# Kernel tuning notes

Hardware: AMD Instinct MI355X
Metric: run time of the kernel (lower is better)

The kernel has to match this reference:

```python
import jax, jax.numpy as jnp
import numpy as np

N = 50000      # nodes
DEG = 16       # fixed neighbors per node
F = 128        # feat_dim
E = N * DEG    # edges
EPS = 1e-12


def setup_inputs() -> dict:
    key = jax.random.key(0)
    k_x, k_col = jax.random.split(key)
    x = jax.random.normal(k_x, (N, F), dtype=jnp.float32)
    col_id = jax.random.randint(k_col, (E,), 0, N, dtype=jnp.int32)
    row_ptr = (jnp.arange(N + 1, dtype=jnp.int32) * DEG)          # CSR offsets, fixed degree
    row_id = jnp.repeat(jnp.arange(N, dtype=jnp.int32), DEG)      # COO row index per edge
    beta = jnp.ones((1,), dtype=jnp.float32)
    return {"x": x, "row_id": row_id, "row_ptr": row_ptr, "col_id": col_id, "beta": beta}


def reference(x, row_id, row_ptr, col_id, beta):
    # AGNN: alpha_ij = softmax_j( beta * cos(x_i, x_j) ), out_i = sum_j alpha_ij * x_j
    n = x.shape[0]
    xn = x * jax.lax.rsqrt(jnp.sum(x * x, axis=-1, keepdims=True) + EPS)   # row-normalized
    # per-edge cosine similarity scaled by beta
    e = beta[0] * jnp.sum(xn[row_id] * xn[col_id], axis=-1)                # [E]
    # segment softmax over each row's neighborhood
    m = jax.ops.segment_max(e, row_id, num_segments=n)                      # [N]
    ee = jnp.exp(e - m[row_id])
    s = jax.ops.segment_sum(ee, row_id, num_segments=n)                     # [N]
    alpha = ee / s[row_id]                                                  # [E]
    # attention-weighted aggregation of raw neighbor features
    out = jax.ops.segment_sum(alpha[:, None] * x[col_id], row_id, num_segments=n)  # [N, F]
    return out
```

## Files before the change

kernel.cpp:

```cpp
#include <hip/hip_runtime.h>
#include <math.h>
#include <stdint.h>

#define DEG 16
#define FDIM 128
#define EPSV 1e-12f

__device__ __forceinline__ uint32_t f32_to_bf16_rne(float f) {
    uint32_t u = __float_as_uint(f);
    return (u + 0x7fffu + ((u >> 16) & 1u)) >> 16;
}

__device__ __forceinline__ void unpack8(const uint4 u, float* f) {
    f[0] = __uint_as_float(u.x << 16); f[1] = __uint_as_float(u.x & 0xffff0000u);
    f[2] = __uint_as_float(u.y << 16); f[3] = __uint_as_float(u.y & 0xffff0000u);
    f[4] = __uint_as_float(u.z << 16); f[5] = __uint_as_float(u.z & 0xffff0000u);
    f[6] = __uint_as_float(u.w << 16); f[7] = __uint_as_float(u.w & 0xffff0000u);
}

__global__ void agnn_prep_kernel(const float* __restrict__ x,
                                 uint32_t* __restrict__ xbf,
                                 float* __restrict__ rn, int n) {
    int wave = (blockIdx.x * blockDim.x + threadIdx.x) >> 6;
    int lane = threadIdx.x & 63;
    if (wave >= n) return;
    const float2 v = *reinterpret_cast<const float2*>(x + (size_t)wave * FDIM + lane * 2);
    float s = v.x * v.x + v.y * v.y;
#pragma unroll
    for (int off = 32; off >= 1; off >>= 1)
        s += __shfl_xor(s, off);
    if (lane == 0) rn[wave] = rsqrtf(s + EPSV);
    xbf[(size_t)wave * (FDIM / 2) + lane] =
        f32_to_bf16_rne(v.x) | (f32_to_bf16_rne(v.y) << 16);
}

__global__ void agnn_main_v3(const uint32_t* __restrict__ xbf,
                             const int* __restrict__ col_id,
                             const float* __restrict__ rn,
                             const float* __restrict__ beta,
                             float* __restrict__ out, int n) {
    int wave = (blockIdx.x * blockDim.x + threadIdx.x) >> 6;
    int lane = threadIdx.x & 63;
    if (wave >= n) return;
    const int node = wave;
    const int g = lane >> 4;
    const int t = lane & 15;

    const float b   = beta[0];
    const float rni = rn[node];

    const uint4 xiu = *reinterpret_cast<const uint4*>(xbf + (size_t)node * (FDIM / 2) + t * 4);
    float xi[8];
    unpack8(xiu, xi);

    const int call = col_id[node * DEG + t];

    int   cj[4];
    uint4 xju[4];
#pragma unroll
    for (int r = 0; r < 4; ++r) {
        cj[r]  = __shfl(call, 4 * g + r);
        xju[r] = *reinterpret_cast<const uint4*>(xbf + (size_t)cj[r] * (FDIM / 2) + t * 4);
    }
    float rnj[4];
#pragma unroll
    for (int r = 0; r < 4; ++r) rnj[r] = rn[cj[r]];

    float p[4];
#pragma unroll
    for (int r = 0; r < 4; ++r) {
        float xv[8];
        unpack8(xju[r], xv);
        float d0 = xi[0] * xv[0];
        float d1 = xi[1] * xv[1];
#pragma unroll
        for (int q = 2; q < 8; q += 2) {
            d0 = fmaf(xi[q],     xv[q],     d0);
            d1 = fmaf(xi[q + 1], xv[q + 1], d1);
        }
        p[r] = d0 + d1;
    }

#pragma unroll
    for (int off = 1; off < 16; off <<= 1) {
#pragma unroll
        for (int r = 0; r < 4; ++r)
            p[r] += __shfl_xor(p[r], off);
    }

    const float brni = b * rni;
#pragma unroll
    for (int r = 0; r < 4; ++r)
        p[r] *= brni * rnj[r];

    float m = fmaxf(fmaxf(p[0], p[1]), fmaxf(p[2], p[3]));
    m = fmaxf(m, __shfl_xor(m, 16));
    m = fmaxf(m, __shfl_xor(m, 32));
    float s = 0.f;
#pragma unroll
    for (int r = 0; r < 4; ++r) { p[r] = __expf(p[r] - m); s += p[r]; }
    s += __shfl_xor(s, 16);
    s += __shfl_xor(s, 32);
    const float inv = 1.0f / s;

    float acc[8] = {0.f, 0.f, 0.f, 0.f, 0.f, 0.f, 0.f, 0.f};
#pragma unroll
    for (int r = 0; r < 4; ++r) {
        const float a = p[r] * inv;
        float xv[8];
        unpack8(xju[r], xv);
#pragma unroll
        for (int q = 0; q < 8; ++q)
            acc[q] = fmaf(a, xv[q], acc[q]);
    }
#pragma unroll
    for (int q = 0; q < 8; ++q) acc[q] += __shfl_xor(acc[q], 16);
#pragma unroll
    for (int q = 0; q < 8; ++q) acc[q] += __shfl_xor(acc[q], 32);

    if (g == 0) {
        float4* op = reinterpret_cast<float4*>(out + (size_t)node * FDIM + t * 8);
        op[0] = make_float4(acc[0], acc[1], acc[2], acc[3]);
        op[1] = make_float4(acc[4], acc[5], acc[6], acc[7]);
    }
}

__global__ void agnn_rnorm_kernel(const float* __restrict__ x,
                                  float* __restrict__ rn, int n) {
    int wave = (blockIdx.x * blockDim.x + threadIdx.x) >> 6;
    int lane = threadIdx.x & 63;
    if (wave >= n) return;
    const float2 v = *reinterpret_cast<const float2*>(x + (size_t)wave * FDIM + lane * 2);
    float s = v.x * v.x + v.y * v.y;
#pragma unroll
    for (int off = 32; off >= 1; off >>= 1)
        s += __shfl_xor(s, off);
    if (lane == 0) rn[wave] = rsqrtf(s + EPSV);
}

__global__ void agnn_main_f32(const float* __restrict__ x,
                              const int* __restrict__ col_id,
                              const float* __restrict__ rn,
                              const float* __restrict__ beta,
                              float* __restrict__ out, int n) {
    int wave = (blockIdx.x * blockDim.x + threadIdx.x) >> 6;
    int lane = threadIdx.x & 63;
    if (wave >= n) return;
    const int node = wave;
    const float b   = beta[0];
    const float rni = rn[node];
    const float2 xi = *reinterpret_cast<const float2*>(x + (size_t)node * FDIM + lane * 2);
    int cidx = col_id[node * DEG + (lane & 15)];
    float2 xj[DEG];
    float  p[DEG];
    float  rnj[DEG];
#pragma unroll
    for (int k = 0; k < DEG; ++k) {
        int cj = __shfl(cidx, k);
        const float2 v = *reinterpret_cast<const float2*>(x + (size_t)cj * FDIM + lane * 2);
        xj[k] = v; rnj[k] = rn[cj];
        p[k] = fmaf(xi.x, v.x, xi.y * v.y);
    }
#pragma unroll
    for (int off = 32; off >= 1; off >>= 1) {
#pragma unroll
        for (int k = 0; k < DEG; ++k)
            p[k] += __shfl_xor(p[k], off);
    }
    const float brni = b * rni;
#pragma unroll
    for (int k = 0; k < DEG; ++k) p[k] *= brni * rnj[k];
    float m = p[0];
#pragma unroll
    for (int k = 1; k < DEG; ++k) m = fmaxf(m, p[k]);
    float s = 0.f;
#pragma unroll
    for (int k = 0; k < DEG; ++k) { p[k] = __expf(p[k] - m); s += p[k]; }
    const float inv = 1.0f / s;
    float2 acc = make_float2(0.f, 0.f);
#pragma unroll
    for (int k = 0; k < DEG; ++k) {
        const float a = p[k] * inv;
        acc.x = fmaf(a, xj[k].x, acc.x);
        acc.y = fmaf(a, xj[k].y, acc.y);
    }
    *reinterpret_cast<float2*>(out + (size_t)node * FDIM + lane * 2) = acc;
}

extern "C" void kernel_launch(void* const* d_in, const int* in_sizes, int n_in,
                              void* d_out, int out_size, void* d_ws, size_t ws_size,
                              hipStream_t stream) {
    const float* x      = (const float*)d_in[0];
    const int*   col_id = (const int*)d_in[3];
    const float* beta   = (const float*)d_in[4];
    float*       out    = (float*)d_out;

    const int n = in_sizes[0] / FDIM;

    const int block = 256;
    const int wavesPerBlock = block / 64;
    const int grid = (n + wavesPerBlock - 1) / wavesPerBlock;

    const size_t xbf_bytes = (size_t)n * (FDIM / 2) * sizeof(uint32_t);
    const size_t need = xbf_bytes + (size_t)n * sizeof(float);

    if (ws_size >= need) {
        uint32_t* xbf = (uint32_t*)d_ws;
        float*    rn  = (float*)((char*)d_ws + xbf_bytes);
        agnn_prep_kernel<<<grid, block, 0, stream>>>(x, xbf, rn, n);
        agnn_main_v3<<<grid, block, 0, stream>>>(xbf, col_id, rn, beta, out, n);
    } else {
        float* rn = (float*)d_ws;
        agnn_rnorm_kernel<<<grid, block, 0, stream>>>(x, rn, n);
        agnn_main_f32<<<grid, block, 0, stream>>>(x, col_id, rn, beta, out, n);
    }
}
```

Baseline: 44.04 us.

## Process two nodes per wave with vectorized index loads and max-free softmax

Result: no change. 44.46 us (+1.0%).

```diff
diff --git a/kernel.cpp b/kernel.cpp
--- a/kernel.cpp
+++ b/kernel.cpp
@@ -18,6 +18,19 @@
     f[6] = __uint_as_float(u.w << 16); f[7] = __uint_as_float(u.w & 0xffff0000u);
 }
 
+__device__ __forceinline__ float dot8(const float* xi, const uint4 u) {
+    float xv[8];
+    unpack8(u, xv);
+    float d0 = xi[0] * xv[0];
+    float d1 = xi[1] * xv[1];
+#pragma unroll
+    for (int q = 2; q < 8; q += 2) {
+        d0 = fmaf(xi[q],     xv[q],     d0);
+        d1 = fmaf(xi[q + 1], xv[q + 1], d1);
+    }
+    return d0 + d1;
+}
+
 __global__ void agnn_prep_kernel(const float* __restrict__ x,
                                  uint32_t* __restrict__ xbf,
                                  float* __restrict__ rn, int n) {
@@ -34,94 +47,118 @@
         f32_to_bf16_rne(v.x) | (f32_to_bf16_rne(v.y) << 16);
 }
 
-__global__ void agnn_main_v3(const uint32_t* __restrict__ xbf,
-                             const int* __restrict__ col_id,
-                             const float* __restrict__ rn,
-                             const float* __restrict__ beta,
-                             float* __restrict__ out, int n) {
-    int wave = (blockIdx.x * blockDim.x + threadIdx.x) >> 6;
-    int lane = threadIdx.x & 63;
-    if (wave >= n) return;
-    const int node = wave;
+__global__ __launch_bounds__(256, 4)
+void agnn_main_v5(const uint32_t* __restrict__ xbf,
+                  const int* __restrict__ col_id,
+                  const float* __restrict__ rn,
+                  const float* __restrict__ beta,
+                  float* __restrict__ out, int n) {
+    int wid  = (blockIdx.x * blockDim.x + threadIdx.x) >> 6;
+    int lane = threadIdx.x & 63;
+    const int nA = 2 * wid;
+    if (nA >= n) return;
+    const int nB = (nA + 1 < n) ? (nA + 1) : nA;
     const int g = lane >> 4;
     const int t = lane & 15;
 
-    const float b   = beta[0];
-    const float rni = rn[node];
-
-    const uint4 xiu = *reinterpret_cast<const uint4*>(xbf + (size_t)node * (FDIM / 2) + t * 4);
-    float xi[8];
-    unpack8(xiu, xi);
-
-    const int call = col_id[node * DEG + t];
-
-    int   cj[4];
-    uint4 xju[4];
-#pragma unroll
-    for (int r = 0; r < 4; ++r) {
-        cj[r]  = __shfl(call, 4 * g + r);
-        xju[r] = *reinterpret_cast<const uint4*>(xbf + (size_t)cj[r] * (FDIM / 2) + t * 4);
-    }
-    float rnj[4];
-#pragma unroll
-    for (int r = 0; r < 4; ++r) rnj[r] = rn[cj[r]];
-
-    float p[4];
-#pragma unroll
-    for (int r = 0; r < 4; ++r) {
-        float xv[8];
-        unpack8(xju[r], xv);
-        float d0 = xi[0] * xv[0];
-        float d1 = xi[1] * xv[1];
-#pragma unroll
-        for (int q = 2; q < 8; q += 2) {
-            d0 = fmaf(xi[q],     xv[q],     d0);
-            d1 = fmaf(xi[q + 1], xv[q + 1], d1);
+    const int4  cA = *reinterpret_cast<const int4*>(col_id + nA * DEG + 4 * g);
+    const int4  cB = *reinterpret_cast<const int4*>(col_id + nB * DEG + 4 * g);
+    const uint4 xiuA = *reinterpret_cast<const uint4*>(xbf + (size_t)nA * (FDIM / 2) + t * 4);
+    const uint4 xiuB = *reinterpret_cast<const uint4*>(xbf + (size_t)nB * (FDIM / 2) + t * 4);
+    const float b    = beta[0];
+    const float rniA = rn[nA];
+    const float rniB = rn[nB];
+
+    uint4 a0 = *reinterpret_cast<const uint4*>(xbf + (size_t)cA.x * (FDIM / 2) + t * 4);
+    uint4 a1 = *reinterpret_cast<const uint4*>(xbf + (size_t)cA.y * (FDIM / 2) + t * 4);
+    uint4 a2 = *reinterpret_cast<const uint4*>(xbf + (size_t)cA.z * (FDIM / 2) + t * 4);
+    uint4 a3 = *reinterpret_cast<const uint4*>(xbf + (size_t)cA.w * (FDIM / 2) + t * 4);
+    uint4 b0 = *reinterpret_cast<const uint4*>(xbf + (size_t)cB.x * (FDIM / 2) + t * 4);
+    uint4 b1 = *reinterpret_cast<const uint4*>(xbf + (size_t)cB.y * (FDIM / 2) + t * 4);
+    uint4 b2 = *reinterpret_cast<const uint4*>(xbf + (size_t)cB.z * (FDIM / 2) + t * 4);
+    uint4 b3 = *reinterpret_cast<const uint4*>(xbf + (size_t)cB.w * (FDIM / 2) + t * 4);
+
+    float rnjA0 = rn[cA.x], rnjA1 = rn[cA.y], rnjA2 = rn[cA.z], rnjA3 = rn[cA.w];
+    float rnjB0 = rn[cB.x], rnjB1 = rn[cB.y], rnjB2 = rn[cB.z], rnjB3 = rn[cB.w];
+
+    float xiA[8], xiB[8];
+    unpack8(xiuA, xiA);
+    unpack8(xiuB, xiB);
+
+    float pA[4], pB[4];
+    pA[0] = dot8(xiA, a0); pB[0] = dot8(xiB, b0);
+    pA[1] = dot8(xiA, a1); pB[1] = dot8(xiB, b1);
+    pA[2] = dot8(xiA, a2); pB[2] = dot8(xiB, b2);
+    pA[3] = dot8(xiA, a3); pB[3] = dot8(xiB, b3);
+
+#pragma unroll
+    for (int off = 1; off < 16; off <<= 1) {
+#pragma unroll
+        for (int r = 0; r < 4; ++r) {
+            pA[r] += __shfl_xor(pA[r], off);
+            pB[r] += __shfl_xor(pB[r], off);
         }
-        p[r] = d0 + d1;
-    }
-
-#pragma unroll
-    for (int off = 1; off < 16; off <<= 1) {
-#pragma unroll
-        for (int r = 0; r < 4; ++r)
-            p[r] += __shfl_xor(p[r], off);
-    }
-
-    const float brni = b * rni;
-#pragma unroll
-    for (int r = 0; r < 4; ++r)
-        p[r] *= brni * rnj[r];
-
-    float m = fmaxf(fmaxf(p[0], p[1]), fmaxf(p[2], p[3]));
-    m = fmaxf(m, __shfl_xor(m, 16));
-    m = fmaxf(m, __shfl_xor(m, 32));
-    float s = 0.f;
-#pragma unroll
-    for (int r = 0; r < 4; ++r) { p[r] = __expf(p[r] - m); s += p[r]; }
-    s += __shfl_xor(s, 16);
-    s += __shfl_xor(s, 32);
-    const float inv = 1.0f / s;
-
-    float acc[8] = {0.f, 0.f, 0.f, 0.f, 0.f, 0.f, 0.f, 0.f};
-#pragma unroll
-    for (int r = 0; r < 4; ++r) {
-        const float a = p[r] * inv;
-        float xv[8];
-        unpack8(xju[r], xv);
-#pragma unroll
-        for (int q = 0; q < 8; ++q)
-            acc[q] = fmaf(a, xv[q], acc[q]);
-    }
-#pragma unroll
-    for (int q = 0; q < 8; ++q) acc[q] += __shfl_xor(acc[q], 16);
-#pragma unroll
-    for (int q = 0; q < 8; ++q) acc[q] += __shfl_xor(acc[q], 32);
+    }
+
+    const float bA = b * rniA, bB = b * rniB;
+    pA[0] = __expf(pA[0] * (bA * rnjA0));
+    pA[1] = __expf(pA[1] * (bA * rnjA1));
+    pA[2] = __expf(pA[2] * (bA * rnjA2));
+    pA[3] = __expf(pA[3] * (bA * rnjA3));
+    pB[0] = __expf(pB[0] * (bB * rnjB0));
+    pB[1] = __expf(pB[1] * (bB * rnjB1));
+    pB[2] = __expf(pB[2] * (bB * rnjB2));
+    pB[3] = __expf(pB[3] * (bB * rnjB3));
+
+    float sA = (pA[0] + pA[1]) + (pA[2] + pA[3]);
+    float sB = (pB[0] + pB[1]) + (pB[2] + pB[3]);
+    sA += __shfl_xor(sA, 16);  sB += __shfl_xor(sB, 16);
+    sA += __shfl_xor(sA, 32);  sB += __shfl_xor(sB, 32);
+    const float invA = 1.0f / sA;
+    const float invB = 1.0f / sB;
+
+    float accA[8], accB[8];
+    {
+        float xv[8], w;
+        unpack8(a0, xv); w = pA[0] * invA;
+#pragma unroll
+        for (int q = 0; q < 8; ++q) accA[q] = w * xv[q];
+        unpack8(a1, xv); w = pA[1] * invA;
+#pragma unroll
+        for (int q = 0; q < 8; ++q) accA[q] = fmaf(w, xv[q], accA[q]);
+        unpack8(a2, xv); w = pA[2] * invA;
+#pragma unroll
+        for (int q = 0; q < 8; ++q) accA[q] = fmaf(w, xv[q], accA[q]);
+        unpack8(a3, xv); w = pA[3] * invA;
+#pragma unroll
+        for (int q = 0; q < 8; ++q) accA[q] = fmaf(w, xv[q], accA[q]);
+
+        unpack8(b0, xv); w = pB[0] * invB;
+#pragma unroll
+        for (int q = 0; q < 8; ++q) accB[q] = w * xv[q];
+        unpack8(b1, xv); w = pB[1] * invB;
+#pragma unroll
+        for (int q = 0; q < 8; ++q) accB[q] = fmaf(w, xv[q], accB[q]);
+        unpack8(b2, xv); w = pB[2] * invB;
+#pragma unroll
+        for (int q = 0; q < 8; ++q) accB[q] = fmaf(w, xv[q], accB[q]);
+        unpack8(b3, xv); w = pB[3] * invB;
+#pragma unroll
+        for (int q = 0; q < 8; ++q) accB[q] = fmaf(w, xv[q], accB[q]);
+    }
+
+#pragma unroll
+    for (int q = 0; q < 8; ++q) { accA[q] += __shfl_xor(accA[q], 16); accB[q] += __shfl_xor(accB[q], 16); }
+#pragma unroll
+    for (int q = 0; q < 8; ++q) { accA[q] += __shfl_xor(accA[q], 32); accB[q] += __shfl_xor(accB[q], 32); }
 
     if (g == 0) {
-        float4* op = reinterpret_cast<float4*>(out + (size_t)node * FDIM + t * 8);
-        op[0] = make_float4(acc[0], acc[1], acc[2], acc[3]);
-        op[1] = make_float4(acc[4], acc[5], acc[6], acc[7]);
+        float4* opA = reinterpret_cast<float4*>(out + (size_t)nA * FDIM + t * 8);
+        opA[0] = make_float4(accA[0], accA[1], accA[2], accA[3]);
+        opA[1] = make_float4(accA[4], accA[5], accA[6], accA[7]);
+        float4* opB = reinterpret_cast<float4*>(out + (size_t)nB * FDIM + t * 8);
+        opB[0] = make_float4(accB[0], accB[1], accB[2], accB[3]);
+        opB[1] = make_float4(accB[4], accB[5], accB[6], accB[7]);
     }
 }
 
@@ -199,7 +236,7 @@
 
     const int block = 256;
     const int wavesPerBlock = block / 64;
-    const int grid = (n + wavesPerBlock - 1) / wavesPerBlock;
+    const int gridPrep = (n + wavesPerBlock - 1) / wavesPerBlock;
 
     const size_t xbf_bytes = (size_t)n * (FDIM / 2) * sizeof(uint32_t);
     const size_t need = xbf_bytes + (size_t)n * sizeof(float);
@@ -207,11 +244,13 @@
     if (ws_size >= need) {
         uint32_t* xbf = (uint32_t*)d_ws;
         float*    rn  = (float*)((char*)d_ws + xbf_bytes);
-        agnn_prep_kernel<<<grid, block, 0, stream>>>(x, xbf, rn, n);
-        agnn_main_v3<<<grid, block, 0, stream>>>(xbf, col_id, rn, beta, out, n);
+        const int nPairs   = (n + 1) / 2;
+        const int gridMain = (nPairs + wavesPerBlock - 1) / wavesPerBlock;
+        agnn_prep_kernel<<<gridPrep, block, 0, stream>>>(x, xbf, rn, n);
+        agnn_main_v5<<<gridMain, block, 0, stream>>>(xbf, col_id, rn, beta, out, n);
     } else {
         float* rn = (float*)d_ws;
-        agnn_rnorm_kernel<<<grid, block, 0, stream>>>(x, rn, n);
-        agnn_main_f32<<<grid, block, 0, stream>>>(x, col_id, rn, beta, out, n);
-    }
-}
+        agnn_rnorm_kernel<<<gridPrep, block, 0, stream>>>(x, rn, n);
+        agnn_main_f32<<<gridPrep, block, 0, stream>>>(x, col_id, rn, beta, out, n);
+    }
+}
```
